# Kernel optimization log

Hardware: AMD Instinct MI355X
Metric: run time of the kernel (lower is better)

## Reference

```python
import jax, jax.numpy as jnp
import numpy as np

B, L, SH, EH, A, T = 128, 200, 512, 512, 512, 3


def setup_inputs() -> dict:
    key = jax.random.key(0)
    ks = jax.random.split(key, 13)
    s = 0.05  # small init scale to keep tanh/sigmoid unsaturated
    return {
        "sent_enc_doc": jax.random.normal(ks[0], (B, L, 2 * SH), jnp.float32),
        "h0_w": jax.random.normal(ks[1], (EH, SH), jnp.float32) * s,
        "h0_b": jax.random.normal(ks[2], (EH,), jnp.float32) * s,
        "gru_w_ih": jax.random.normal(ks[3], (3 * EH, 2 * SH), jnp.float32) * s,
        "gru_w_hh": jax.random.normal(ks[4], (3 * EH, EH), jnp.float32) * s,
        "gru_b_ih": jax.random.normal(ks[5], (3 * EH,), jnp.float32) * s,
        "gru_b_hh": jax.random.normal(ks[6], (3 * EH,), jnp.float32) * s,
        "wq": jax.random.normal(ks[7], (A, EH), jnp.float32) * s,
        "bq": jax.random.normal(ks[8], (A,), jnp.float32) * s,
        "wd": jax.random.normal(ks[9], (A, 2 * SH), jnp.float32) * s,
        "bd": jax.random.normal(ks[10], (A,), jnp.float32) * s,
        "ws": jax.random.normal(ks[11], (1, A), jnp.float32) * s,
        "bs": jax.random.normal(ks[12], (1,), jnp.float32) * s,
    }


def reference(sent_enc_doc, h0_w, h0_b, gru_w_ih, gru_w_hh, gru_b_ih, gru_b_hh,
              wq, bq, wd, bd, ws, bs):
    b, l, d2 = sent_enc_doc.shape
    sh = d2 // 2
    eh = gru_w_hh.shape[1]
    neg = jnp.asarray(-1e6, sent_enc_doc.dtype)

    # h0 = tanh(W * last backward vector), replicated across doc_len
    last_back = sent_enc_doc[:, 0, sh:]                      # (B, SH)
    h0 = jnp.tanh(last_back @ h0_w.T + h0_b)                 # (B, EH)
    h = jnp.broadcast_to(h0[:, None, :], (b, l, eh))         # (B, L, EH)

    s_prev = jnp.zeros((b, l, d2), sent_enc_doc.dtype)
    d_proj = sent_enc_doc @ wd.T + bd                        # (B, L, A) - loop-invariant
    mask = jnp.zeros((b, l), bool)
    rows = jnp.arange(b)

    scores_list, sel_list = [], []
    for _ in range(T):  # fixed, tiny, sequentially-dependent loop
        # GRUCell (torch gate order: r, z, n)
        gx = s_prev @ gru_w_ih.T + gru_b_ih                  # (B, L, 3EH)
        gh = h @ gru_w_hh.T + gru_b_hh                       # (B, L, 3EH)
        xr, xz, xn = jnp.split(gx, 3, axis=-1)
        hr, hz, hn = jnp.split(gh, 3, axis=-1)
        r = jax.nn.sigmoid(xr + hr)
        z = jax.nn.sigmoid(xz + hz)
        n = jnp.tanh(xn + r * hn)
        h = (1.0 - z) * n + z * h                            # (B, L, EH)

        # scorer: ws . tanh(Wq h + Wd s_i)
        score = (jnp.tanh(h @ wq.T + bq + d_proj) @ ws.T + bs)[..., 0]  # (B, L)
        score = jnp.where(mask, neg, score)
        idx = jnp.argmax(score, axis=1)                      # (B,)
        mask = mask.at[rows, idx].set(True)

        # gather the selected sentence encoding, broadcast to all positions
        s_sel = jnp.take_along_axis(sent_enc_doc, idx[:, None, None], axis=1)  # (B,1,2SH)
        s_prev = jnp.broadcast_to(s_sel, (b, l, d2))

        scores_list.append(score)
        sel_list.append(idx)

    sents_scores = jnp.stack(scores_list, axis=1)            # (B, T, L)
    sents_selected = jnp.stack(sel_list, axis=1)             # (B, T)
    return sents_scores, sents_selected
```

## Files before the change

### kernel.cpp

```cpp
#include <hip/hip_runtime.h>
#include <hip/hip_bf16.h>

constexpr int Bn  = 128;
constexpr int Ln  = 200;
constexpr int D2n = 1024;
constexpr int G3n = 1536;
constexpr int Tn  = 3;
constexpr int Nn  = 512;
constexpr int Kn  = 1024;

typedef unsigned short ushort;
typedef float f32x4 __attribute__((ext_vector_type(4)));
typedef __bf16 bf16x8 __attribute__((ext_vector_type(8)));

__device__ __forceinline__ ushort f2bf(float f) {
  unsigned u = __float_as_uint(f);
  unsigned r = (u + 0x7fffu + ((u >> 16) & 1u)) >> 16;
  return (ushort)r;
}
__device__ __forceinline__ float bf2f(ushort h) {
  return __uint_as_float(((unsigned)h) << 16);
}

__device__ __forceinline__ void gld_lds16(const ushort* g, ushort* l) {
  __builtin_amdgcn_global_load_lds(
      (const __attribute__((address_space(1))) unsigned int*)g,
      (__attribute__((address_space(3))) unsigned int*)l, 16, 0, 0);
}

__device__ __forceinline__ float ftanh(float x) {
  float cx = fminf(fmaxf(x, -15.f), 15.f);
  float e  = __expf(2.f * cx);
  return (e - 1.f) * __builtin_amdgcn_rcpf(e + 1.f);
}

__global__ void k_split(const float* __restrict__ W, ushort* __restrict__ hi,
                        ushort* __restrict__ lo) {
  int i = blockIdx.x * 256 + threadIdx.x;
  float4 v = ((const float4*)W)[i];
  ushort4 h, l;
  h.x = f2bf(v.x); l.x = f2bf(v.x - bf2f(h.x));
  h.y = f2bf(v.y); l.y = f2bf(v.y - bf2f(h.y));
  h.z = f2bf(v.z); l.z = f2bf(v.z - bf2f(h.z));
  h.w = f2bf(v.w); l.w = f2bf(v.w - bf2f(h.w));
  ((ushort4*)hi)[i] = h;
  ((ushort4*)lo)[i] = l;
}

__global__ void k_split3(const float* __restrict__ w_ih, const float* __restrict__ w_hh,
                         const float* __restrict__ wq,
                         ushort* __restrict__ WihH, ushort* __restrict__ WihL,
                         ushort* __restrict__ WhhH, ushort* __restrict__ WhhL,
                         ushort* __restrict__ WqH, ushort* __restrict__ WqL) {
  int i = blockIdx.x * 256 + threadIdx.x;
  const float* src; ushort* hi; ushort* lo; int off;
  if (i < 393216)      { src = w_ih; hi = WihH; lo = WihL; off = i; }
  else if (i < 589824) { src = w_hh; hi = WhhH; lo = WhhL; off = i - 393216; }
  else                 { src = wq;   hi = WqH;  lo = WqL;  off = i - 589824; }
  float4 v = ((const float4*)src)[off];
  ushort4 h, l;
  h.x = f2bf(v.x); l.x = f2bf(v.x - bf2f(h.x));
  h.y = f2bf(v.y); l.y = f2bf(v.y - bf2f(h.y));
  h.z = f2bf(v.z); l.z = f2bf(v.z - bf2f(h.z));
  h.w = f2bf(v.w); l.w = f2bf(v.w - bf2f(h.w));
  ((ushort4*)hi)[off] = h;
  ((ushort4*)lo)[off] = l;
}

__launch_bounds__(256)
__global__ void k_h0(const float* __restrict__ sent, const float* __restrict__ W,
                     const float* __restrict__ bias, float* __restrict__ out,
                     ushort* __restrict__ outh, ushort* __restrict__ outl) {
  __shared__ float s[16 * 512];
  const int b0 = blockIdx.y * 16;
  const int jl = threadIdx.x & 63;
  const int j  = blockIdx.x * 64 + jl;
  const int bg = (threadIdx.x >> 6) * 4;

  for (int i = threadIdx.x; i < 2048; i += 256) {
    int r = i >> 7, c = i & 127;
    ((float4*)s)[i] = *(const float4*)(sent + (size_t)(b0 + r) * (Ln * D2n) + 512 + c * 4);
  }
  __syncthreads();

  const float4* w4 = (const float4*)(W + (size_t)j * 512);
  const float4* r0 = (const float4*)(s + (size_t)(bg + 0) * 512);
  const float4* r1 = (const float4*)(s + (size_t)(bg + 1) * 512);
  const float4* r2 = (const float4*)(s + (size_t)(bg + 2) * 512);
  const float4* r3 = (const float4*)(s + (size_t)(bg + 3) * 512);

  float acc0 = 0.f, acc1 = 0.f, acc2 = 0.f, acc3 = 0.f;
  #pragma unroll 4
  for (int k4 = 0; k4 < 128; ++k4) {
    float4 wv = w4[k4];
    float4 a;
    a = r0[k4]; acc0 += wv.x*a.x + wv.y*a.y + wv.z*a.z + wv.w*a.w;
    a = r1[k4]; acc1 += wv.x*a.x + wv.y*a.y + wv.z*a.z + wv.w*a.w;
    a = r2[k4]; acc2 += wv.x*a.x + wv.y*a.y + wv.z*a.z + wv.w*a.w;
    a = r3[k4]; acc3 += wv.x*a.x + wv.y*a.y + wv.z*a.z + wv.w*a.w;
  }
  float bb = bias[j];
  float accs[4] = {acc0, acc1, acc2, acc3};
  #pragma unroll
  for (int i = 0; i < 4; ++i) {
    float v = tanhf(accs[i] + bb);
    size_t o = (size_t)(b0 + bg + i) * 512 + j;
    out[o] = v;
    ushort hv = f2bf(v);
    outh[o] = hv;
    outl[o] = f2bf(v - bf2f(hv));
  }
}

template<int KK>
__device__ __forceinline__ void mfma_tile128(
    const ushort* __restrict__ Ah, const ushort* __restrict__ Al,
    const ushort* __restrict__ Bh, const ushort* __restrict__ Bl,
    const float* __restrict__ bias, float* __restrict__ C, int ldc,
    int m0, int n0) {
  __shared__ __align__(16) ushort sAh[128 * 32];
  __shared__ __align__(16) ushort sAl[128 * 32];
  __shared__ __align__(16) ushort sBh[128 * 32];
  __shared__ __align__(16) ushort sBl[128 * 32];

  const int tid  = threadIdx.x;
  const int wave = tid >> 6, lane = tid & 63;
  const int wy = (wave >> 1) * 64, wx = (wave & 1) * 64;
  const int lm = lane & 15, lq = lane >> 4;
  const int fs = (lq ^ ((lm >> 1) & 3)) * 8;

  const int S0 = (wave * 2 + 0) * 64 + lane;
  const int S1 = (wave * 2 + 1) * 64 + lane;
  const int r0 = S0 >> 2, r1 = S1 >> 2;
  const int c0 = ((S0 & 3) ^ ((r0 >> 1) & 3)) * 8;
  const int c1 = ((S1 & 3) ^ ((r1 >> 1) & 3)) * 8;
  const ushort* pAh0 = Ah + (size_t)(m0 + r0) * KK + c0;
  const ushort* pAh1 = Ah + (size_t)(m0 + r1) * KK + c1;
  const ushort* pAl0 = Al + (size_t)(m0 + r0) * KK + c0;
  const ushort* pAl1 = Al + (size_t)(m0 + r1) * KK + c1;
  const ushort* pBh0 = Bh + (size_t)(n0 + r0) * KK + c0;
  const ushort* pBh1 = Bh + (size_t)(n0 + r1) * KK + c1;
  const ushort* pBl0 = Bl + (size_t)(n0 + r0) * KK + c0;
  const ushort* pBl1 = Bl + (size_t)(n0 + r1) * KK + c1;
  ushort* dA0 = &sAh[S0 * 8]; ushort* dA1 = &sAh[S1 * 8];
  ushort* dL0 = &sAl[S0 * 8]; ushort* dL1 = &sAl[S1 * 8];
  ushort* dB0 = &sBh[S0 * 8]; ushort* dB1 = &sBh[S1 * 8];
  ushort* dC0 = &sBl[S0 * 8]; ushort* dC1 = &sBl[S1 * 8];

  f32x4 acc[4][4] = {};

  for (int ks = 0; ks < KK / 32; ++ks) {
    const int ko = ks * 32;
    gld_lds16(pAh0 + ko, dA0); gld_lds16(pAh1 + ko, dA1);
    gld_lds16(pAl0 + ko, dL0); gld_lds16(pAl1 + ko, dL1);
    gld_lds16(pBh0 + ko, dB0); gld_lds16(pBh1 + ko, dB1);
    gld_lds16(pBl0 + ko, dC0); gld_lds16(pBl1 + ko, dC1);
    __syncthreads();

    bf16x8 ah[4], al[4], bh[4], bl[4];
    #pragma unroll
    for (int mi = 0; mi < 4; ++mi) {
      const int o = (wy + mi * 16 + lm) * 32 + fs;
      ah[mi] = *(const bf16x8*)&sAh[o];
      al[mi] = *(const bf16x8*)&sAl[o];
    }
    #pragma unroll
    for (int ni = 0; ni < 4; ++ni) {
      const int o = (wx + ni * 16 + lm) * 32 + fs;
      bh[ni] = *(const bf16x8*)&sBh[o];
      bl[ni] = *(const bf16x8*)&sBl[o];
    }
    #pragma unroll
    for (int mi = 0; mi < 4; ++mi)
      #pragma unroll
      for (int ni = 0; ni < 4; ++ni) {
        acc[mi][ni] = __builtin_amdgcn_mfma_f32_16x16x32_bf16(ah[mi], bh[ni], acc[mi][ni], 0, 0, 0);
        acc[mi][ni] = __builtin_amdgcn_mfma_f32_16x16x32_bf16(ah[mi], bl[ni], acc[mi][ni], 0, 0, 0);
        acc[mi][ni] = __builtin_amdgcn_mfma_f32_16x16x32_bf16(al[mi], bh[ni], acc[mi][ni], 0, 0, 0);
      }
    __syncthreads();
  }

  #pragma unroll
  for (int ni = 0; ni < 4; ++ni) {
    int col = n0 + wx + ni * 16 + lm;
    float bb = bias[col];
    #pragma unroll
    for (int mi = 0; mi < 4; ++mi) {
      int rbase = m0 + wy + mi * 16 + lq * 4;
      #pragma unroll
      for (int r = 0; r < 4; ++r)
        C[(size_t)(rbase + r) * ldc + col] = acc[mi][ni][r] + bb;
    }
  }
}

__launch_bounds__(256)
__global__ void k_dproj_mfma(const ushort* __restrict__ Ahi, const ushort* __restrict__ Alo,
                             const ushort* __restrict__ Whi, const ushort* __restrict__ Wlo,
                             const float* __restrict__ bias, float* __restrict__ C) {
  const int bid = blockIdx.x;
  mfma_tile128<1024>(Ahi, Alo, Whi, Wlo, bias, C, Nn, (bid % 200) * 128, (bid / 200) * 128);
}

__launch_bounds__(256)
__global__ void k_q_mfma(const ushort* __restrict__ hh, const ushort* __restrict__ hl,
                         const ushort* __restrict__ WqH, const ushort* __restrict__ WqL,
                         const float* __restrict__ bq, float* __restrict__ q) {
  mfma_tile128<512>(hh, hl, WqH, WqL, bq, q, 512, 0, blockIdx.x * 128);
}

__launch_bounds__(256)
__global__ void k_gates(const ushort* __restrict__ sxh, const ushort* __restrict__ sxl,
                        const float* __restrict__ hOld,
                        const ushort* __restrict__ hh, const ushort* __restrict__ hl,
                        const ushort* __restrict__ WihH, const ushort* __restrict__ WihL,
                        const ushort* __restrict__ WhhH, const ushort* __restrict__ WhhL,
                        const float* __restrict__ b_ih, const float* __restrict__ b_hh,
                        float* __restrict__ hNew, ushort* __restrict__ hhN,
                        ushort* __restrict__ hlN) {
  __shared__ __align__(16) ushort sAh[2][64 * 32];
  __shared__ __align__(16) ushort sAl[2][64 * 32];
  __shared__ __align__(16) ushort sWh[2][48 * 32];
  __shared__ __align__(16) ushort sWl[2][48 * 32];

  const int bb  = blockIdx.x >> 5;
  const int j0  = (blockIdx.x & 31) * 16;
  const int rb0 = bb * 64;
  const int tid = threadIdx.x, wave = tid >> 6, lane = tid & 63;
  const int wy = wave * 16;
  const int lm = lane & 15, lq = lane >> 4;
  const int fs = (lq ^ ((lm >> 1) & 3)) * 8;

  const int rA = tid >> 2;
  const int cA = ((tid & 3) ^ ((rA >> 1) & 3)) * 8;
  const bool wOn = tid < 192;
  const int gw = (rA >> 4) * 512 + j0 + (rA & 15);

  f32x4 ax[3] = {};
  f32x4 ag[3] = {};

  for (int ks = 0; ks < 16; ++ks) {
    const int ko = ks * 64;
    #pragma unroll
    for (int kk = 0; kk < 2; ++kk) {
      gld_lds16(sxh + (size_t)(rb0 + rA) * 1024 + ko + kk * 32 + cA, &sAh[kk][tid * 8]);
      gld_lds16(sxl + (size_t)(rb0 + rA) * 1024 + ko + kk * 32 + cA, &sAl[kk][tid * 8]);
      if (wOn) {
        gld_lds16(WihH + (size_t)gw * 1024 + ko + kk * 32 + cA, &sWh[kk][tid * 8]);
        gld_lds16(WihL + (size_t)gw * 1024 + ko + kk * 32 + cA, &sWl[kk][tid * 8]);
      }
    }
    __syncthreads();
    #pragma unroll
    for (int kk = 0; kk < 2; ++kk) {
      const int oA = (wy + lm) * 32 + fs;
      bf16x8 fah = *(const bf16x8*)&sAh[kk][oA];
      bf16x8 fal = *(const bf16x8*)&sAl[kk][oA];
      #pragma unroll
      for (int g = 0; g < 3; ++g) {
        const int oW = (g * 16 + lm) * 32 + fs;
        bf16x8 fbh = *(const bf16x8*)&sWh[kk][oW];
        bf16x8 fbl = *(const bf16x8*)&sWl[kk][oW];
        ax[g] = __builtin_amdgcn_mfma_f32_16x16x32_bf16(fah, fbh, ax[g], 0, 0, 0);
        ax[g] = __builtin_amdgcn_mfma_f32_16x16x32_bf16(fah, fbl, ax[g], 0, 0, 0);
        ax[g] = __builtin_amdgcn_mfma_f32_16x16x32_bf16(fal, fbh, ax[g], 0, 0, 0);
      }
    }
    __syncthreads();
  }

  for (int ks = 0; ks < 8; ++ks) {
    const int ko = ks * 64;
    #pragma unroll
    for (int kk = 0; kk < 2; ++kk) {
      gld_lds16(hh + (size_t)(rb0 + rA) * 512 + ko + kk * 32 + cA, &sAh[kk][tid * 8]);
      gld_lds16(hl + (size_t)(rb0 + rA) * 512 + ko + kk * 32 + cA, &sAl[kk][tid * 8]);
      if (wOn) {
        gld_lds16(WhhH + (size_t)gw * 512 + ko + kk * 32 + cA, &sWh[kk][tid * 8]);
        gld_lds16(WhhL + (size_t)gw * 512 + ko + kk * 32 + cA, &sWl[kk][tid * 8]);
      }
    }
    __syncthreads();
    #pragma unroll
    for (int kk = 0; kk < 2; ++kk) {
      const int oA = (wy + lm) * 32 + fs;
      bf16x8 fah = *(const bf16x8*)&sAh[kk][oA];
      bf16x8 fal = *(const bf16x8*)&sAl[kk][oA];
      #pragma unroll
      for (int g = 0; g < 3; ++g) {
        const int oW = (g * 16 + lm) * 32 + fs;
        bf16x8 fbh = *(const bf16x8*)&sWh[kk][oW];
        bf16x8 fbl = *(const bf16x8*)&sWl[kk][oW];
        ag[g] = __builtin_amdgcn_mfma_f32_16x16x32_bf16(fah, fbh, ag[g], 0, 0, 0);
        ag[g] = __builtin_amdgcn_mfma_f32_16x16x32_bf16(fah, fbl, ag[g], 0, 0, 0);
        ag[g] = __builtin_amdgcn_mfma_f32_16x16x32_bf16(fal, fbh, ag[g], 0, 0, 0);
      }
    }
    __syncthreads();
  }

  const int j = j0 + lm;
  const float bir = b_ih[j], biz = b_ih[512 + j], bin = b_ih[1024 + j];
  const float bhr = b_hh[j], bhz = b_hh[512 + j], bhn = b_hh[1024 + j];
  #pragma unroll
  for (int rr = 0; rr < 4; ++rr) {
    const int b = rb0 + wy + lq * 4 + rr;
    float xr = ax[0][rr] + bir, hr = ag[0][rr] + bhr;
    float xz = ax[1][rr] + biz, hz = ag[1][rr] + bhz;
    float xn = ax[2][rr] + bin, hn = ag[2][rr] + bhn;
    float r = 1.f / (1.f + expf(-(xr + hr)));
    float z = 1.f / (1.f + expf(-(xz + hz)));
    float n = tanhf(xn + r * hn);
    float hv = hOld[(size_t)b * 512 + j];
    float hw = (1.f - z) * n + z * hv;
    hNew[(size_t)b * 512 + j] = hw;
    ushort hbf = f2bf(hw);
    hhN[(size_t)b * 512 + j] = hbf;
    hlN[(size_t)b * 512 + j] = f2bf(hw - bf2f(hbf));
  }
}

__launch_bounds__(256)
__global__ void k_score_argmax(const float* __restrict__ dproj, const float* __restrict__ q,
                               const float* __restrict__ wsv, const float* __restrict__ bsv,
                               const float* __restrict__ sent,
                               ushort* __restrict__ s_rowh, ushort* __restrict__ s_rowl,
                               int* __restrict__ mask, float* __restrict__ outScores,
                               float* __restrict__ outSel, int t) {
  const int b = blockIdx.x;
  const int tid = threadIdx.x, lane = tid & 63, wv = tid >> 6;
  __shared__ float ssc[Ln];
  __shared__ int s_idx;

  const float4* q4  = (const float4*)(q + (size_t)b * Nn);
  const float4* ws4 = (const float4*)wsv;
  const float4 qq0 = q4[lane],  qq1 = q4[lane + 64];
  const float4 wv0 = ws4[lane], wv1 = ws4[lane + 64];
  const float bs0 = bsv[0];

  for (int l = wv; l < Ln; l += 4) {
    const float4* dp4 = (const float4*)(dproj + ((size_t)b * Ln + l) * Nn);
    float4 d0 = dp4[lane], d1 = dp4[lane + 64];
    float sum = ftanh(qq0.x + d0.x) * wv0.x + ftanh(qq0.y + d0.y) * wv0.y
              + ftanh(qq0.z + d0.z) * wv0.z + ftanh(qq0.w + d0.w) * wv0.w
              + ftanh(qq1.x + d1.x) * wv1.x + ftanh(qq1.y + d1.y) * wv1.y
              + ftanh(qq1.z + d1.z) * wv1.z + ftanh(qq1.w + d1.w) * wv1.w;
    #pragma unroll
    for (int off = 32; off > 0; off >>= 1) sum += __shfl_xor(sum, off, 64);
    if (lane == 0) {
      float v = sum + bs0;
      if (mask[b * Ln + l]) v = -1000000.0f;
      ssc[l] = v;
      outScores[(size_t)b * (Tn * Ln) + t * Ln + l] = v;
    }
  }
  __syncthreads();

  if (tid < 64) {
    float best = -3.0e38f; int bi = 0;
    for (int l = tid; l < Ln; l += 64) {
      float v = ssc[l];
      if (v > best) { best = v; bi = l; }
    }
    #pragma unroll
    for (int off = 32; off > 0; off >>= 1) {
      float ov = __shfl_down(best, off, 64);
      int   oi = __shfl_down(bi,   off, 64);
      if (ov > best || (ov == best && oi < bi)) { best = ov; bi = oi; }
    }
    if (tid == 0) s_idx = bi;
  }
  __syncthreads();
  int idx = s_idx;
  const float* src = sent + ((size_t)b * Ln + idx) * D2n;
  int k = tid * 4;
  float4 v = *(const float4*)(src + k);
  ushort4 hvec, lvec;
  hvec.x = f2bf(v.x); lvec.x = f2bf(v.x - bf2f(hvec.x));
  hvec.y = f2bf(v.y); lvec.y = f2bf(v.y - bf2f(hvec.y));
  hvec.z = f2bf(v.z); lvec.z = f2bf(v.z - bf2f(hvec.z));
  hvec.w = f2bf(v.w); lvec.w = f2bf(v.w - bf2f(hvec.w));
  *(ushort4*)(s_rowh + (size_t)b * 1024 + k) = hvec;
  *(ushort4*)(s_rowl + (size_t)b * 1024 + k) = lvec;
  if (tid == 0) {
    mask[b * Ln + idx] = 1;
    outSel[(size_t)b * Tn + t] = (float)idx;
  }
}

extern "C" void kernel_launch(void* const* d_in, const int* in_sizes, int n_in,
                              void* d_out, int out_size, void* d_ws, size_t ws_size,
                              hipStream_t stream) {
  const float* sent = (const float*)d_in[0];
  const float* h0_w = (const float*)d_in[1];
  const float* h0_b = (const float*)d_in[2];
  const float* w_ih = (const float*)d_in[3];
  const float* w_hh = (const float*)d_in[4];
  const float* b_ih = (const float*)d_in[5];
  const float* b_hh = (const float*)d_in[6];
  const float* wq   = (const float*)d_in[7];
  const float* bq   = (const float*)d_in[8];
  const float* wd   = (const float*)d_in[9];
  const float* bd   = (const float*)d_in[10];
  const float* wsv  = (const float*)d_in[11];
  const float* bsv  = (const float*)d_in[12];

  float* wsf     = (float*)d_ws;
  float* d_proj  = wsf;
  float* hA      = d_proj + 13107200;
  float* hB      = hA + 65536;
  float* q       = hB + 65536;
  int*   mask    = (int*)(q + 65536);
  ushort* Whi    = (ushort*)(mask + 25600);
  ushort* Wlo    = Whi + 524288;
  ushort* hhA    = Wlo + 524288;
  ushort* hlA    = hhA + 65536;
  ushort* hhB    = hlA + 65536;
  ushort* hlB    = hhB + 65536;
  ushort* s_rowh = hlB + 65536;
  ushort* s_rowl = s_rowh + 131072;
  ushort* Ahi    = s_rowl + 131072;
  ushort* Alo    = Ahi + 26214400;

  ushort* WihH   = Ahi;
  ushort* WihL   = WihH + 1572864;
  ushort* WhhH   = WihL + 1572864;
  ushort* WhhL   = WhhH + 786432;
  ushort* WqH    = WhhL + 786432;
  ushort* WqL    = WqH + 262144;

  float* outScores = (float*)d_out;
  float* outSel    = outScores + (size_t)Bn * Tn * Ln;

  hipMemsetAsync(mask, 0, 25600 * sizeof(int), stream);
  hipMemsetAsync(s_rowh, 0, 2 * 131072 * sizeof(ushort), stream);

  k_h0<<<dim3(8, 8), 256, 0, stream>>>(sent, h0_w, h0_b, hA, hhA, hlA);
  k_split<<<512,   256, 0, stream>>>(wd, Whi, Wlo);
  k_split<<<25600, 256, 0, stream>>>(sent, Ahi, Alo);
  k_dproj_mfma<<<800, 256, 0, stream>>>(Ahi, Alo, Whi, Wlo, bd, d_proj);
  k_split3<<<2560, 256, 0, stream>>>(w_ih, w_hh, wq, WihH, WihL, WhhH, WhhL, WqH, WqL);

  float* hc = hA;  ushort* hhc = hhA; ushort* hlc = hlA;
  float* hn = hB;  ushort* hhn = hhB; ushort* hln = hlB;
  for (int t = 0; t < Tn; ++t) {
    k_gates<<<64, 256, 0, stream>>>(s_rowh, s_rowl, hc, hhc, hlc,
                                    WihH, WihL, WhhH, WhhL, b_ih, b_hh,
                                    hn, hhn, hln);
    k_q_mfma<<<4, 256, 0, stream>>>(hhn, hln, WqH, WqL, bq, q);
    k_score_argmax<<<128, 256, 0, stream>>>(d_proj, q, wsv, bsv, sent,
                                            s_rowh, s_rowl, mask,
                                            outScores, outSel, t);
    float* tf = hc; hc = hn; hn = tf;
    ushort* t1 = hhc; hhc = hhn; hhn = t1;
    ushort* t2 = hlc; hlc = hln; hln = t2;
  }
}
```

Measured before the change: 570.0 us.

## Fuse query projection into score kernel and double-buffer GRU gate loads

Drops the separate 4-block MFMA kernel for q = Wq·h. Each score block now computes its own row of q in fp32 from a transposed Wq, which saves one launch per step and removes the tiny low-occupancy GEMM. It also double-buffers the LDS staging in the GRU gate kernel so global loads for the next K-slice overlap the MFMAs on the current one. The cost is that every one of the 128 score blocks reads the full 1 MB Wq, and the gate kernel uses twice the shared memory.

```diff
diff --git a/kernel.cpp b/kernel.cpp
--- a/kernel.cpp
+++ b/kernel.cpp
@@ -48,15 +48,12 @@
 }
 
 __global__ void k_split3(const float* __restrict__ w_ih, const float* __restrict__ w_hh,
-                         const float* __restrict__ wq,
                          ushort* __restrict__ WihH, ushort* __restrict__ WihL,
-                         ushort* __restrict__ WhhH, ushort* __restrict__ WhhL,
-                         ushort* __restrict__ WqH, ushort* __restrict__ WqL) {
+                         ushort* __restrict__ WhhH, ushort* __restrict__ WhhL) {
   int i = blockIdx.x * 256 + threadIdx.x;
   const float* src; ushort* hi; ushort* lo; int off;
-  if (i < 393216)      { src = w_ih; hi = WihH; lo = WihL; off = i; }
-  else if (i < 589824) { src = w_hh; hi = WhhH; lo = WhhL; off = i - 393216; }
-  else                 { src = wq;   hi = WqH;  lo = WqL;  off = i - 589824; }
+  if (i < 393216) { src = w_ih; hi = WihH; lo = WihL; off = i; }
+  else            { src = w_hh; hi = WhhH; lo = WhhL; off = i - 393216; }
   float4 v = ((const float4*)src)[off];
   ushort4 h, l;
   h.x = f2bf(v.x); l.x = f2bf(v.x - bf2f(h.x));
@@ -65,6 +62,20 @@
   h.w = f2bf(v.w); l.w = f2bf(v.w - bf2f(h.w));
   ((ushort4*)hi)[off] = h;
   ((ushort4*)lo)[off] = l;
+}
+
+__global__ void k_transp(const float* __restrict__ in, float* __restrict__ out,
+                         int R, int C) {
+  __shared__ float t[32][33];
+  const int x = threadIdx.x, y = threadIdx.y;
+  const int c0 = blockIdx.x * 32, r0 = blockIdx.y * 32;
+  #pragma unroll
+  for (int i = 0; i < 4; ++i)
+    t[y + i * 8][x] = in[(size_t)(r0 + y + i * 8) * C + c0 + x];
+  __syncthreads();
+  #pragma unroll
+  for (int i = 0; i < 4; ++i)
+    out[(size_t)(c0 + y + i * 8) * R + r0 + x] = t[x][y + i * 8];
 }
 
 __launch_bounds__(256)
@@ -204,13 +215,6 @@
 }
 
 __launch_bounds__(256)
-__global__ void k_q_mfma(const ushort* __restrict__ hh, const ushort* __restrict__ hl,
-                         const ushort* __restrict__ WqH, const ushort* __restrict__ WqL,
-                         const float* __restrict__ bq, float* __restrict__ q) {
-  mfma_tile128<512>(hh, hl, WqH, WqL, bq, q, 512, 0, blockIdx.x * 128);
-}
-
-__launch_bounds__(256)
 __global__ void k_gates(const ushort* __restrict__ sxh, const ushort* __restrict__ sxl,
                         const float* __restrict__ hOld,
                         const ushort* __restrict__ hh, const ushort* __restrict__ hl,
@@ -219,10 +223,10 @@
                         const float* __restrict__ b_ih, const float* __restrict__ b_hh,
                         float* __restrict__ hNew, ushort* __restrict__ hhN,
                         ushort* __restrict__ hlN) {
-  __shared__ __align__(16) ushort sAh[2][64 * 32];
-  __shared__ __align__(16) ushort sAl[2][64 * 32];
-  __shared__ __align__(16) ushort sWh[2][48 * 32];
-  __shared__ __align__(16) ushort sWl[2][48 * 32];
+  __shared__ __align__(16) ushort sAh[2][2][64 * 32];
+  __shared__ __align__(16) ushort sAl[2][2][64 * 32];
+  __shared__ __align__(16) ushort sWh[2][2][48 * 32];
+  __shared__ __align__(16) ushort sWl[2][2][48 * 32];
 
   const int bb  = blockIdx.x >> 5;
   const int j0  = (blockIdx.x & 31) * 16;
@@ -237,67 +241,72 @@
   const bool wOn = tid < 192;
   const int gw = (rA >> 4) * 512 + j0 + (rA & 15);
 
+  const ushort* sxh_r = sxh + (size_t)(rb0 + rA) * 1024 + cA;
+  const ushort* sxl_r = sxl + (size_t)(rb0 + rA) * 1024 + cA;
+  const ushort* hh_r  = hh  + (size_t)(rb0 + rA) * 512  + cA;
+  const ushort* hl_r  = hl  + (size_t)(rb0 + rA) * 512  + cA;
+  const ushort* wih_h = WihH + (size_t)gw * 1024 + cA;
+  const ushort* wih_l = WihL + (size_t)gw * 1024 + cA;
+  const ushort* whh_h = WhhH + (size_t)gw * 512 + cA;
+  const ushort* whh_l = WhhL + (size_t)gw * 512 + cA;
+
+  auto stage = [&](int s, int buf) {
+    if (s < 16) {
+      const int ko = s * 64;
+      #pragma unroll
+      for (int kk = 0; kk < 2; ++kk) {
+        gld_lds16(sxh_r + ko + kk * 32, &sAh[buf][kk][tid * 8]);
+        gld_lds16(sxl_r + ko + kk * 32, &sAl[buf][kk][tid * 8]);
+        if (wOn) {
+          gld_lds16(wih_h + ko + kk * 32, &sWh[buf][kk][tid * 8]);
+          gld_lds16(wih_l + ko + kk * 32, &sWl[buf][kk][tid * 8]);
+        }
+      }
+    } else {
+      const int ko = (s - 16) * 64;
+      #pragma unroll
+      for (int kk = 0; kk < 2; ++kk) {
+        gld_lds16(hh_r + ko + kk * 32, &sAh[buf][kk][tid * 8]);
+        gld_lds16(hl_r + ko + kk * 32, &sAl[buf][kk][tid * 8]);
+        if (wOn) {
+          gld_lds16(whh_h + ko + kk * 32, &sWh[buf][kk][tid * 8]);
+          gld_lds16(whh_l + ko + kk * 32, &sWl[buf][kk][tid * 8]);
+        }
+      }
+    }
+  };
+
   f32x4 ax[3] = {};
   f32x4 ag[3] = {};
 
-  for (int ks = 0; ks < 16; ++ks) {
-    const int ko = ks * 64;
+  auto compute = [&](int cur, f32x4 (&acc)[3]) {
+    const int oA = (wy + lm) * 32 + fs;
     #pragma unroll
     for (int kk = 0; kk < 2; ++kk) {
-      gld_lds16(sxh + (size_t)(rb0 + rA) * 1024 + ko + kk * 32 + cA, &sAh[kk][tid * 8]);
-      gld_lds16(sxl + (size_t)(rb0 + rA) * 1024 + ko + kk * 32 + cA, &sAl[kk][tid * 8]);
-      if (wOn) {
-        gld_lds16(WihH + (size_t)gw * 1024 + ko + kk * 32 + cA, &sWh[kk][tid * 8]);
-        gld_lds16(WihL + (size_t)gw * 1024 + ko + kk * 32 + cA, &sWl[kk][tid * 8]);
-      }
-    }
-    __syncthreads();
-    #pragma unroll
-    for (int kk = 0; kk < 2; ++kk) {
-      const int oA = (wy + lm) * 32 + fs;
-      bf16x8 fah = *(const bf16x8*)&sAh[kk][oA];
-      bf16x8 fal = *(const bf16x8*)&sAl[kk][oA];
+      bf16x8 fah = *(const bf16x8*)&sAh[cur][kk][oA];
+      bf16x8 fal = *(const bf16x8*)&sAl[cur][kk][oA];
       #pragma unroll
       for (int g = 0; g < 3; ++g) {
         const int oW = (g * 16 + lm) * 32 + fs;
-        bf16x8 fbh = *(const bf16x8*)&sWh[kk][oW];
-        bf16x8 fbl = *(const bf16x8*)&sWl[kk][oW];
-        ax[g] = __builtin_amdgcn_mfma_f32_16x16x32_bf16(fah, fbh, ax[g], 0, 0, 0);
-        ax[g] = __builtin_amdgcn_mfma_f32_16x16x32_bf16(fah, fbl, ax[g], 0, 0, 0);
-        ax[g] = __builtin_amdgcn_mfma_f32_16x16x32_bf16(fal, fbh, ax[g], 0, 0, 0);
+        bf16x8 fbh = *(const bf16x8*)&sWh[cur][kk][oW];
+        bf16x8 fbl = *(const bf16x8*)&sWl[cur][kk][oW];
+        acc[g] = __builtin_amdgcn_mfma_f32_16x16x32_bf16(fah, fbh, acc[g], 0, 0, 0);
+        acc[g] = __builtin_amdgcn_mfma_f32_16x16x32_bf16(fah, fbl, acc[g], 0, 0, 0);
+        acc[g] = __builtin_amdgcn_mfma_f32_16x16x32_bf16(fal, fbh, acc[g], 0, 0, 0);
       }
     }
+  };
+
+  stage(0, 0);
+  asm volatile("s_waitcnt vmcnt(0)" ::: "memory");
+
+  for (int s = 0; s < 24; ++s) {
+    const int cur = s & 1, nxt = cur ^ 1;
     __syncthreads();
-  }
-
-  for (int ks = 0; ks < 8; ++ks) {
-    const int ko = ks * 64;
-    #pragma unroll
-    for (int kk = 0; kk < 2; ++kk) {
-      gld_lds16(hh + (size_t)(rb0 + rA) * 512 + ko + kk * 32 + cA, &sAh[kk][tid * 8]);
-      gld_lds16(hl + (size_t)(rb0 + rA) * 512 + ko + kk * 32 + cA, &sAl[kk][tid * 8]);
-      if (wOn) {
-        gld_lds16(WhhH + (size_t)gw * 512 + ko + kk * 32 + cA, &sWh[kk][tid * 8]);
-        gld_lds16(WhhL + (size_t)gw * 512 + ko + kk * 32 + cA, &sWl[kk][tid * 8]);
-      }
-    }
-    __syncthreads();
-    #pragma unroll
-    for (int kk = 0; kk < 2; ++kk) {
-      const int oA = (wy + lm) * 32 + fs;
-      bf16x8 fah = *(const bf16x8*)&sAh[kk][oA];
-      bf16x8 fal = *(const bf16x8*)&sAl[kk][oA];
-      #pragma unroll
-      for (int g = 0; g < 3; ++g) {
-        const int oW = (g * 16 + lm) * 32 + fs;
-        bf16x8 fbh = *(const bf16x8*)&sWh[kk][oW];
-        bf16x8 fbl = *(const bf16x8*)&sWl[kk][oW];
-        ag[g] = __builtin_amdgcn_mfma_f32_16x16x32_bf16(fah, fbh, ag[g], 0, 0, 0);
-        ag[g] = __builtin_amdgcn_mfma_f32_16x16x32_bf16(fah, fbl, ag[g], 0, 0, 0);
-        ag[g] = __builtin_amdgcn_mfma_f32_16x16x32_bf16(fal, fbh, ag[g], 0, 0, 0);
-      }
-    }
-    __syncthreads();
+    if (s + 1 < 24) stage(s + 1, nxt);
+    if (s < 16) compute(cur, ax); else compute(cur, ag);
+    if (s + 1 < 24)
+      asm volatile("s_waitcnt vmcnt(0)" ::: "memory");
   }
 
   const int j = j0 + lm;
@@ -322,7 +331,8 @@
 }
 
 __launch_bounds__(256)
-__global__ void k_score_argmax(const float* __restrict__ dproj, const float* __restrict__ q,
+__global__ void k_score_argmax(const float* __restrict__ dproj, const float* __restrict__ h,
+                               const float* __restrict__ wqT, const float* __restrict__ bq,
                                const float* __restrict__ wsv, const float* __restrict__ bsv,
                                const float* __restrict__ sent,
                                ushort* __restrict__ s_rowh, ushort* __restrict__ s_rowl,
@@ -330,10 +340,27 @@
                                float* __restrict__ outSel, int t) {
   const int b = blockIdx.x;
   const int tid = threadIdx.x, lane = tid & 63, wv = tid >> 6;
+  __shared__ float shb[512];
+  __shared__ float sq[512];
   __shared__ float ssc[Ln];
   __shared__ int s_idx;
 
-  const float4* q4  = (const float4*)(q + (size_t)b * Nn);
+  if (tid < 128)
+    ((float4*)shb)[tid] = ((const float4*)(h + (size_t)b * 512))[tid];
+  __syncthreads();
+
+  float qx = 0.f, qy = 0.f;
+  #pragma unroll 8
+  for (int k = 0; k < 512; ++k) {
+    float hk = shb[k];
+    float2 w = ((const float2*)(wqT + (size_t)k * 512))[tid];
+    qx += hk * w.x; qy += hk * w.y;
+  }
+  sq[tid * 2]     = qx + bq[tid * 2];
+  sq[tid * 2 + 1] = qy + bq[tid * 2 + 1];
+  __syncthreads();
+
+  const float4* q4  = (const float4*)sq;
   const float4* ws4 = (const float4*)wsv;
   const float4 qq0 = q4[lane],  qq1 = q4[lane + 64];
   const float4 wv0 = ws4[lane], wv1 = ws4[lane + 64];
@@ -410,8 +437,7 @@
   float* d_proj  = wsf;
   float* hA      = d_proj + 13107200;
   float* hB      = hA + 65536;
-  float* q       = hB + 65536;
-  int*   mask    = (int*)(q + 65536);
+  int*   mask    = (int*)(hB + 65536);
   ushort* Whi    = (ushort*)(mask + 25600);
   ushort* Wlo    = Whi + 524288;
   ushort* hhA    = Wlo + 524288;
@@ -427,8 +453,7 @@
   ushort* WihL   = WihH + 1572864;
   ushort* WhhH   = WihL + 1572864;
   ushort* WhhL   = WhhH + 786432;
-  ushort* WqH    = WhhL + 786432;
-  ushort* WqL    = WqH + 262144;
+  float*  wqT    = (float*)(WhhL + 786432);
 
   float* outScores = (float*)d_out;
   float* outSel    = outScores + (size_t)Bn * Tn * Ln;
@@ -440,7 +465,8 @@
   k_split<<<512,   256, 0, stream>>>(wd, Whi, Wlo);
   k_split<<<25600, 256, 0, stream>>>(sent, Ahi, Alo);
   k_dproj_mfma<<<800, 256, 0, stream>>>(Ahi, Alo, Whi, Wlo, bd, d_proj);
-  k_split3<<<2560, 256, 0, stream>>>(w_ih, w_hh, wq, WihH, WihL, WhhH, WhhL, WqH, WqL);
+  k_split3<<<2304, 256, 0, stream>>>(w_ih, w_hh, WihH, WihL, WhhH, WhhL);
+  k_transp<<<dim3(16, 16), dim3(32, 8), 0, stream>>>(wq, wqT, 512, 512);
 
   float* hc = hA;  ushort* hhc = hhA; ushort* hlc = hlA;
   float* hn = hB;  ushort* hhn = hhB; ushort* hln = hlB;
@@ -448,8 +474,7 @@
     k_gates<<<64, 256, 0, stream>>>(s_rowh, s_rowl, hc, hhc, hlc,
                                     WihH, WihL, WhhH, WhhL, b_ih, b_hh,
                                     hn, hhn, hln);
-    k_q_mfma<<<4, 256, 0, stream>>>(hhn, hln, WqH, WqL, bq, q);
-    k_score_argmax<<<128, 256, 0, stream>>>(d_proj, q, wsv, bsv, sent,
+    k_score_argmax<<<128, 256, 0, stream>>>(d_proj, hn, wqT, bq, wsv, bsv, sent,
                                             s_rowh, s_rowl, mask,
                                             outScores, outSel, t);
     float* tf = hc; hc = hn; hn = tf;
```

Result: slower. 596.6 us (+4.7%).
